# Kernel tuning notes

Hardware: AMD Instinct MI355X
Metric: run time of the kernel (lower is better)

Reference implementation:

```python
import jax, jax.numpy as jnp
import numpy as np

CHANNELS = 512
NUM_HEADS = 8
GROUPS = 8
EPS = 1e-5


def setup_inputs() -> dict:
    key = jax.random.key(0)
    ks = jax.random.split(key, 7)
    c = CHANNELS
    x = jax.random.normal(ks[0], (32, c, 32, 32), dtype=jnp.float32)
    norm_scale = 1.0 + 0.02 * jax.random.normal(ks[1], (c,), dtype=jnp.float32)
    norm_bias = 0.02 * jax.random.normal(ks[2], (c,), dtype=jnp.float32)
    qkv_w = jax.random.normal(ks[3], (3 * c, c), dtype=jnp.float32) / np.sqrt(c).astype(np.float32)
    qkv_b = 0.01 * jax.random.normal(ks[4], (3 * c,), dtype=jnp.float32)
    proj_w = jax.random.normal(ks[5], (c, c), dtype=jnp.float32) / np.sqrt(c).astype(np.float32)
    proj_b = 0.01 * jax.random.normal(ks[6], (c,), dtype=jnp.float32)
    return {"x": x, "norm_scale": norm_scale, "norm_bias": norm_bias,
            "qkv_w": qkv_w, "qkv_b": qkv_b, "proj_w": proj_w, "proj_b": proj_b}


def reference(x, norm_scale, norm_bias, qkv_w, qkv_b, proj_w, proj_b):
    b, c, h, w = x.shape
    heads = NUM_HEADS
    d = c // heads  # head dim
    # GroupNorm(8, c): normalize over (c//groups, h, w) per group
    xg = x.reshape(b, GROUPS, -1)
    mean = xg.mean(axis=-1, keepdims=True)
    var = xg.var(axis=-1, keepdims=True)
    xn = ((xg - mean) * jax.lax.rsqrt(var + EPS)).reshape(b, c, h, w)
    xn = xn * norm_scale[:, None, None] + norm_bias[:, None, None]
    # 1x1 conv == per-pixel GEMM over channels
    qkv = jnp.einsum('bchw,oc->bohw', xn, qkv_w) + qkv_b[:, None, None]
    q, k, v = jnp.split(qkv, 3, axis=1)  # each [b, c, h, w]
    q = q.reshape(b, heads, d, h * w)
    k = k.reshape(b, heads, d, h * w)
    v = v.reshape(b, heads, d, h * w)
    # scores: [b, heads, hw, hw]
    attn = jnp.einsum('bhdn,bhdm->bhnm', q, k) * (d ** -0.5)
    attn = jax.nn.softmax(attn, axis=-1)
    out = jnp.einsum('bhnm,bhdm->bhdn', attn, v).reshape(b, c, h, w)
    out = jnp.einsum('bchw,oc->bohw', out, proj_w) + proj_b[:, None, None]
    return out + x
```

## Files before the change

kernel.cpp:

```cpp
#include <hip/hip_runtime.h>
#include <stdint.h>

typedef float  f32x4  __attribute__((ext_vector_type(4)));
typedef float  f32x16 __attribute__((ext_vector_type(16)));
typedef __bf16 bf16x8 __attribute__((ext_vector_type(8)));
typedef unsigned int   u32;
typedef unsigned int   u32x4v __attribute__((ext_vector_type(4)));
typedef unsigned short u16;

#define DEVI static __device__ __forceinline__

DEVI void gload16(void* lds, const void* g) {
  __builtin_amdgcn_global_load_lds((const __attribute__((address_space(1))) u32*)g,
                                   (__attribute__((address_space(3))) u32*)lds, 16, 0, 0);
}
DEVI f32x4 mfma16(bf16x8 a, bf16x8 b, f32x4 c) {
  return __builtin_amdgcn_mfma_f32_16x16x32_bf16(a, b, c, 0, 0, 0);
}
DEVI f32x16 mfma32(bf16x8 a, bf16x8 b, f32x16 c) {
  return __builtin_amdgcn_mfma_f32_32x32x16_bf16(a, b, c, 0, 0, 0);
}
DEVI u16 f2bf(float f) {
  u32 u = __builtin_bit_cast(u32, f);
  return (u16)((u + 0x7FFFu + ((u >> 16) & 1u)) >> 16);
}
DEVI u32 cvtpk(float lo, float hi) {
  u32 r;
  asm("v_cvt_pk_bf16_f32 %0, %1, %2" : "=v"(r) : "v"(lo), "v"(hi));
  return r;
}
DEVI bf16x8 mkfrag(u32 a, u32 b, u32 c, u32 d) {
  u32x4v u = {a, b, c, d};
  return __builtin_bit_cast(bf16x8, u);
}
#if __has_builtin(__builtin_amdgcn_exp2f)
DEVI float exp2fast(float x) { return __builtin_amdgcn_exp2f(x); }
#else
DEVI float exp2fast(float x) { return exp2f(x); }
#endif

__global__ __launch_bounds__(1024) void k_gn_norm_t(
    const float* __restrict__ x, const float* __restrict__ scale,
    const float* __restrict__ bias, u16* __restrict__ xnT) {
  const int g = blockIdx.x, b = blockIdx.y;
  const float* xg = x + ((size_t)(b*8 + g)) * 65536;
  const int t = threadIdx.x;

  float s = 0.f, ss = 0.f;
  const float4* p4 = (const float4*)xg;
  #pragma unroll
  for (int i = 0; i < 16; i++) {
    float4 v = p4[t + i*1024];
    s  += v.x + v.y + v.z + v.w;
    ss += v.x*v.x + v.y*v.y + v.z*v.z + v.w*v.w;
  }
  #pragma unroll
  for (int off = 32; off; off >>= 1) { s += __shfl_down(s, off); ss += __shfl_down(ss, off); }
  __shared__ float sa[16], sb[16];
  __shared__ float stats[2];
  if ((t & 63) == 0) { sa[t >> 6] = s; sb[t >> 6] = ss; }
  __syncthreads();
  if (t == 0) {
    float S = 0.f, SS = 0.f;
    #pragma unroll
    for (int i = 0; i < 16; i++) { S += sa[i]; SS += sb[i]; }
    float mean = S * (1.f/65536.f);
    float var  = SS * (1.f/65536.f) - mean*mean;
    stats[0] = mean;
    stats[1] = rsqrtf(var + 1e-5f);
  }
  __syncthreads();
  const float mean = stats[0], rstd = stats[1];

  __shared__ __align__(16) char T[4][8192];
  const int grp = t >> 8, lt = t & 255;
  const int n_l = lt & 63;
  for (int it = 0; it < 4; it++) {
    const int n0 = (it*4 + grp) * 64;
    #pragma unroll
    for (int i = 0; i < 16; i++) {
      int c_l = i*4 + (lt >> 6);
      float xv = xg[(size_t)c_l*1024 + n0 + n_l];
      float val = (xv - mean)*rstd*scale[g*64 + c_l] + bias[g*64 + c_l];
      *(u16*)(T[grp] + n_l*128 + ((c_l*2) ^ ((n_l&7)<<4))) = f2bf(val);
    }
    __syncthreads();
    u16* outp = xnT + ((size_t)b*1024 + n0)*512 + g*64;
    #pragma unroll
    for (int i = 0; i < 2; i++) {
      int idx = i*256 + lt;
      int n_ = idx >> 3, sl = idx & 7;
      uint4 val = *(const uint4*)(T[grp] + n_*128 + ((sl ^ (n_&7))<<4));
      *(uint4*)((char*)outp + (size_t)n_*1024 + sl*16) = val;
    }
    __syncthreads();
  }
}

__global__ __launch_bounds__(256) void k_cvt(const float* __restrict__ a,
                                             u16* __restrict__ o, int n) {
  int i = blockIdx.x * 256 + threadIdx.x;
  const int stride = gridDim.x * 256;
  for (; i < n; i += stride) o[i] = f2bf(a[i]);
}

template<int MODE>
__global__ __launch_bounds__(256) void k_gemm(
    const u16* __restrict__ A, const u16* __restrict__ Bt,
    const float* __restrict__ bias, const float* __restrict__ xres,
    u16* __restrict__ oq, u16* __restrict__ ok, u16* __restrict__ ov,
    float* __restrict__ out) {
  __shared__ __align__(16) char lds[65536];
  const int t = threadIdx.x;
  const int wv = t >> 6, ln = t & 63;
  const int wr = wv >> 1, wc = wv & 1;
  const int b  = blockIdx.z;
  const int n0 = blockIdx.x * 128;
  const int m0 = blockIdx.y * 128;
  const u16* Bb = Bt + (size_t)b * (1024*512);

  f32x4 acc[4][4];
  #pragma unroll
  for (int i = 0; i < 4; i++)
    #pragma unroll
    for (int j = 0; j < 4; j++) acc[i][j] = f32x4{0.f,0.f,0.f,0.f};

  const int srow = ln >> 3, ssl = ln & 7;
  const int csw  = ssl ^ (srow & 7);

  auto stage = [&](int buf, int kb) {
    char* base = lds + (buf << 15);
    #pragma unroll
    for (int i = 0; i < 4; i++) {
      int row = wv*32 + i*8 + srow;
      gload16(base + (wv*32 + i*8)*128,
              (const char*)A  + ((size_t)(m0+row)*512 + kb*64)*2 + csw*16);
      gload16(base + 16384 + (wv*32 + i*8)*128,
              (const char*)Bb + ((size_t)(n0+row)*512 + kb*64)*2 + csw*16);
    }
  };

  stage(0, 0);
  __syncthreads();

  for (int kb = 0; kb < 8; kb++) {
    if (kb < 7) stage((kb + 1) & 1, kb + 1);
    const char* cb = lds + ((kb & 1) << 15);
    #pragma unroll
    for (int kf = 0; kf < 2; kf++) {
      bf16x8 af[4], bfr[4];
      #pragma unroll
      for (int mi = 0; mi < 4; mi++) {
        int row = wr*64 + mi*16 + (ln & 15);
        af[mi] = *(const bf16x8*)(cb + row*128 + ((kf*64 + ((ln>>4)<<4)) ^ ((row&7)<<4)));
      }
      #pragma unroll
      for (int ni = 0; ni < 4; ni++) {
        int row = wc*64 + ni*16 + (ln & 15);
        bfr[ni] = *(const bf16x8*)(cb + 16384 + row*128 + ((kf*64 + ((ln>>4)<<4)) ^ ((row&7)<<4)));
      }
      __builtin_amdgcn_s_setprio(1);
      #pragma unroll
      for (int mi = 0; mi < 4; mi++)
        #pragma unroll
        for (int ni = 0; ni < 4; ni++)
          acc[mi][ni] = mfma16(af[mi], bfr[ni], acc[mi][ni]);
      __builtin_amdgcn_s_setprio(0);
    }
    __syncthreads();
  }

  if constexpr (MODE == 0) {
    if (m0 >= 1024) {
      #pragma unroll
      for (int mi = 0; mi < 4; mi++) {
        #pragma unroll
        for (int r = 0; r < 4; r++) {
          int o_l = wr*64 + mi*16 + ((ln>>4)<<2) + r;
          float bia = bias[m0 + o_l];
          size_t rowoff = ((size_t)b*512 + (m0-1024) + o_l)*1024 + n0 + wc*64 + (ln & 15);
          #pragma unroll
          for (int ni = 0; ni < 4; ni++)
            ov[rowoff + ni*16] = f2bf(acc[mi][ni][r] + bia);
        }
      }
    } else {
      const bool isq = (m0 < 512);
      const float sq = isq ? 0.18033688f : 1.0f;
      u16* dstb = isq ? oq : ok;
      const int mloc = isq ? m0 : (m0 - 512);
      #pragma unroll
      for (int mi = 0; mi < 4; mi++) {
        #pragma unroll
        for (int r = 0; r < 4; r++) {
          int o_l = wr*64 + mi*16 + ((ln>>4)<<2) + r;
          float bia = bias[m0 + o_l];
          #pragma unroll
          for (int ni = 0; ni < 4; ni++) {
            int n_l = wc*64 + ni*16 + (ln & 15);
            *(u16*)(lds + n_l*256 + ((o_l*2) ^ ((n_l&7)<<4))) =
                f2bf((acc[mi][ni][r] + bia) * sq);
          }
        }
      }
      __syncthreads();
      const int h0 = mloc >> 6;
      #pragma unroll
      for (int i = 0; i < 8; i++) {
        int idx = i*256 + t;
        int n_ = idx >> 4, s = idx & 15;
        uint4 val = *(const uint4*)(lds + n_*256 + ((s ^ (n_&7))<<4));
        u16* dst = dstb + ((size_t)(b*8 + h0 + (s>>3))*1024 + (n0 + n_))*64 + (s&7)*8;
        *(uint4*)dst = val;
      }
    }
  } else {
    #pragma unroll
    for (int mi = 0; mi < 4; mi++) {
      #pragma unroll
      for (int r = 0; r < 4; r++) {
        int o_l = wr*64 + mi*16 + ((ln>>4)<<2) + r;
        float bia = bias[m0 + o_l];
        size_t rowoff = ((size_t)b*512 + m0 + o_l)*1024 + n0 + wc*64 + (ln & 15);
        #pragma unroll
        for (int ni = 0; ni < 4; ni++)
          out[rowoff + ni*16] = acc[mi][ni][r] + bia + xres[rowoff + ni*16];
      }
    }
  }
}

__global__ __launch_bounds__(512, 4) void k_attn(
    const u16* __restrict__ qT, const u16* __restrict__ kT,
    const u16* __restrict__ v, u16* __restrict__ aoT) {
  __shared__ __align__(16) char lds[65536];
  const int t = threadIdx.x, wv = t >> 6, ln = t & 63;
  const int l31 = ln & 31, hi = ln >> 5;
  const int qt = blockIdx.x, h = blockIdx.y, b = blockIdx.z;
  const size_t bh = (size_t)(b*8 + h);
  const int q0 = qt*256 + wv*32;
  const char* qp = (const char*)qT + (bh*1024 + q0)*128;
  const char* kp = (const char*)kT + bh*1024*128;
  const char* vp = (const char*)v  + bh*64*2048;

  const int srow = ln >> 3;
  const int csw16 = ((ln & 7) ^ srow) << 4;
  const int rsw = (l31 & 7) << 4;
  const int grow = wv*8 + srow;

  auto stageChunk = [&](char* base, int mc) {
    gload16(base + wv*1024,         kp + (size_t)(mc*128 + grow)*128 + csw16);
    gload16(base + 8192 + wv*1024,  kp + (size_t)(mc*128 + 64 + grow)*128 + csw16);
    gload16(base + 16384 + wv*1024, vp + (size_t)grow*2048 + mc*256 + csw16);
    gload16(base + 24576 + wv*1024, vp + (size_t)grow*2048 + mc*256 + 128 + csw16);
  };

  stageChunk(lds, 0);

  bf16x8 qf[4];
  #pragma unroll
  for (int ks = 0; ks < 4; ks++)
    qf[ks] = *(const bf16x8*)(qp + (size_t)l31*128 + ks*32 + hi*16);

  f32x16 zv;
  #pragma unroll
  for (int i = 0; i < 16; i++) zv[i] = 0.f;

  f32x16 o0, o1;
  #pragma unroll
  for (int i = 0; i < 16; i++) { o0[i] = 0.f; o1[i] = 0.f; }
  float M = -1e30f, L = 0.f;

  auto qk = [&](const char* Kl, f32x16& s0, f32x16& s1) {
    __builtin_amdgcn_s_setprio(1);
    {
      int col = (hi*16) ^ rsw;
      bf16x8 k0 = *(const bf16x8*)(Kl + (size_t)l31*128 + col);
      bf16x8 k1 = *(const bf16x8*)(Kl + (size_t)(32 + l31)*128 + col);
      s0 = mfma32(k0, qf[0], zv);
      s1 = mfma32(k1, qf[0], zv);
    }
    #pragma unroll
    for (int ks = 1; ks < 4; ks++) {
      int col = (ks*32 + hi*16) ^ rsw;
      bf16x8 k0 = *(const bf16x8*)(Kl + (size_t)l31*128 + col);
      bf16x8 k1 = *(const bf16x8*)(Kl + (size_t)(32 + l31)*128 + col);
      s0 = mfma32(k0, qf[ks], s0);
      s1 = mfma32(k1, qf[ks], s1);
    }
    __builtin_amdgcn_s_setprio(0);
  };

  auto sm = [&](f32x16& s0, f32x16& s1, bf16x8* pf) {
    float m8[8];
    #pragma unroll
    for (int i = 0; i < 8; i++)
      m8[i] = fmaxf(fmaxf(s0[2*i], s0[2*i+1]), fmaxf(s1[2*i], s1[2*i+1]));
    float m4a = fmaxf(m8[0], m8[1]), m4b = fmaxf(m8[2], m8[3]);
    float m4c = fmaxf(m8[4], m8[5]), m4d = fmaxf(m8[6], m8[7]);
    float cm = fmaxf(fmaxf(m4a, m4b), fmaxf(m4c, m4d));
    cm = fmaxf(cm, __shfl_xor(cm, 32));
    if (!__all(cm <= M + 11.f)) {
      float nm = fmaxf(M, cm);
      float al = exp2fast(M - nm);
      M = nm;
      #pragma unroll
      for (int i = 0; i < 16; i++) { o0[i] *= al; o1[i] *= al; }
      L *= al;
    }
    #pragma unroll
    for (int i = 0; i < 16; i++) {
      s0[i] = exp2fast(s0[i] - M);
      s1[i] = exp2fast(s1[i] - M);
    }
    float r8[8];
    #pragma unroll
    for (int i = 0; i < 8; i++)
      r8[i] = (s0[2*i] + s0[2*i+1]) + (s1[2*i] + s1[2*i+1]);
    float r4a = r8[0] + r8[1], r4b = r8[2] + r8[3];
    float r4c = r8[4] + r8[5], r4d = r8[6] + r8[7];
    L += (r4a + r4b) + (r4c + r4d);

    u32 x0 = cvtpk(s0[0],  s0[1]),  x1 = cvtpk(s0[2],  s0[3]);
    u32 x2 = cvtpk(s0[4],  s0[5]),  x3 = cvtpk(s0[6],  s0[7]);
    u32 x4 = cvtpk(s0[8],  s0[9]),  x5 = cvtpk(s0[10], s0[11]);
    u32 x6 = cvtpk(s0[12], s0[13]), x7 = cvtpk(s0[14], s0[15]);
    u32 y0 = cvtpk(s1[0],  s1[1]),  y1 = cvtpk(s1[2],  s1[3]);
    u32 y2 = cvtpk(s1[4],  s1[5]),  y3 = cvtpk(s1[6],  s1[7]);
    u32 y4 = cvtpk(s1[8],  s1[9]),  y5 = cvtpk(s1[10], s1[11]);
    u32 y6 = cvtpk(s1[12], s1[13]), y7 = cvtpk(s1[14], s1[15]);
    u32 e0 = (u32)__shfl_xor((int)(hi ? x0 : x2), 32);
    u32 e1 = (u32)__shfl_xor((int)(hi ? x1 : x3), 32);
    u32 e2 = (u32)__shfl_xor((int)(hi ? x4 : x6), 32);
    u32 e3 = (u32)__shfl_xor((int)(hi ? x5 : x7), 32);
    u32 f0 = (u32)__shfl_xor((int)(hi ? y0 : y2), 32);
    u32 f1 = (u32)__shfl_xor((int)(hi ? y1 : y3), 32);
    u32 f2 = (u32)__shfl_xor((int)(hi ? y4 : y6), 32);
    u32 f3 = (u32)__shfl_xor((int)(hi ? y5 : y7), 32);
    pf[0] = hi ? mkfrag(e0, e1, x2, x3) : mkfrag(x0, x1, e0, e1);
    pf[1] = hi ? mkfrag(e2, e3, x6, x7) : mkfrag(x4, x5, e2, e3);
    pf[2] = hi ? mkfrag(f0, f1, y2, y3) : mkfrag(y0, y1, f0, f1);
    pf[3] = hi ? mkfrag(f2, f3, y6, y7) : mkfrag(y4, y5, f2, f3);
  };

  auto pv = [&](const char* Vl, const bf16x8* pf) {
    __builtin_amdgcn_s_setprio(1);
    #pragma unroll
    for (int s = 0; s < 4; s++) {
      int col = (s*32 + hi*16) ^ rsw;
      bf16x8 v0 = *(const bf16x8*)(Vl + (size_t)l31*128 + col);
      bf16x8 v1 = *(const bf16x8*)(Vl + (size_t)(32 + l31)*128 + col);
      o0 = mfma32(v0, pf[s], o0);
      o1 = mfma32(v1, pf[s], o1);
    }
    __builtin_amdgcn_s_setprio(0);
  };

  __syncthreads();

  for (int mc = 0; mc < 8; mc++) {
    char* cb = lds + ((mc & 1) << 15);
    if (mc < 7) stageChunk(lds + (((mc + 1) & 1) << 15), mc + 1);
    f32x16 sa0, sa1, sb0, sb1;
    bf16x8 pfA[4], pfB[4];
    qk(cb, sa0, sa1);
    sm(sa0, sa1, pfA);
    qk(cb + 8192, sb0, sb1);
    pv(cb + 16384, pfA);
    sm(sb0, sb1, pfB);
    pv(cb + 24576, pfB);
    __syncthreads();
  }

  L += __shfl_xor(L, 32);
  float inv = 1.f / L;
  u16* dst = aoT + ((size_t)(b*1024 + q0 + l31))*512 + h*64;
  #pragma unroll
  for (int qd = 0; qd < 4; qd++) {
    uint2 val;
    val.x = cvtpk(o0[4*qd+0]*inv, o0[4*qd+1]*inv);
    val.y = cvtpk(o0[4*qd+2]*inv, o0[4*qd+3]*inv);
    *(uint2*)(dst + qd*8 + hi*4) = val;
  }
  #pragma unroll
  for (int qd = 0; qd < 4; qd++) {
    uint2 val;
    val.x = cvtpk(o1[4*qd+0]*inv, o1[4*qd+1]*inv);
    val.y = cvtpk(o1[4*qd+2]*inv, o1[4*qd+3]*inv);
    *(uint2*)(dst + 32 + qd*8 + hi*4) = val;
  }
}

extern "C" void kernel_launch(void* const* d_in, const int* in_sizes, int n_in,
                              void* d_out, int out_size, void* d_ws, size_t ws_size,
                              hipStream_t stream) {
  const float* x     = (const float*)d_in[0];
  const float* nsc   = (const float*)d_in[1];
  const float* nbi   = (const float*)d_in[2];
  const float* qkvw  = (const float*)d_in[3];
  const float* qkvb  = (const float*)d_in[4];
  const float* projw = (const float*)d_in[5];
  const float* projb = (const float*)d_in[6];
  float* out = (float*)d_out;

  char* ws = (char*)d_ws;
  u16* qkvwb  = (u16*)(ws + 2048);
  u16* projwb = (u16*)(ws + 2048 + 1572864);
  char* p = ws + 2048 + 1572864 + 524288;
  u16* qT  = (u16*)p; p += 33554432;
  u16* kTb = (u16*)p; p += 33554432;
  u16* vb  = (u16*)p; p += 33554432;
  u16* xnT = (u16*)p;
  u16* aoT = xnT;

  k_cvt<<<768, 256, 0, stream>>>(qkvw, qkvwb, 1536*512);
  k_cvt<<<256, 256, 0, stream>>>(projw, projwb, 512*512);
  k_gn_norm_t<<<dim3(8, 32), 1024, 0, stream>>>(x, nsc, nbi, xnT);
  k_gemm<0><<<dim3(8, 12, 32), 256, 0, stream>>>(qkvwb, xnT, qkvb, nullptr,
                                                 qT, kTb, vb, nullptr);
  k_attn<<<dim3(4, 8, 32), 512, 0, stream>>>(qT, kTb, vb, aoT);
  k_gemm<1><<<dim3(8, 4, 32), 256, 0, stream>>>(projwb, aoT, projb, x,
                                                nullptr, nullptr, nullptr, out);
}
```

Measured before the change: 236.9 us.

## Merge weight conversion launches, reorder attention grid, precompute LDS offsets

Folds the two weight fp32-to-bf16 conversion kernels into one launch to cut launch overhead. Remaps the attention grid so that blocks sharing the same batch-head are scheduled far apart rather than adjacent (query tile now on the slow grid axis), which changes L2 locality of the K/V reads. Hoists the swizzled LDS row and column offsets out of the QK and PV loops and unrolls those loops by hand. Most of this mirrors what the compiler probably already did, so the main effects are one fewer launch and different block ordering.

```diff
diff --git a/kernel.cpp b/kernel.cpp
--- a/kernel.cpp
+++ b/kernel.cpp
@@ -97,11 +97,16 @@
   }
 }
 
-__global__ __launch_bounds__(256) void k_cvt(const float* __restrict__ a,
-                                             u16* __restrict__ o, int n) {
+__global__ __launch_bounds__(256) void k_cvt2(const float* __restrict__ a1,
+                                              u16* __restrict__ o1, int n1,
+                                              const float* __restrict__ a2,
+                                              u16* __restrict__ o2, int n2) {
   int i = blockIdx.x * 256 + threadIdx.x;
   const int stride = gridDim.x * 256;
-  for (; i < n; i += stride) o[i] = f2bf(a[i]);
+  for (; i < n1 + n2; i += stride) {
+    if (i < n1) o1[i] = f2bf(a1[i]);
+    else        o2[i - n1] = f2bf(a2[i - n1]);
+  }
 }
 
 template<int MODE>
@@ -236,7 +241,8 @@
   __shared__ __align__(16) char lds[65536];
   const int t = threadIdx.x, wv = t >> 6, ln = t & 63;
   const int l31 = ln & 31, hi = ln >> 5;
-  const int qt = blockIdx.x, h = blockIdx.y, b = blockIdx.z;
+  const int bhi = blockIdx.x, qt = blockIdx.y;
+  const int b = bhi >> 3, h = bhi & 7;
   const size_t bh = (size_t)(b*8 + h);
   const int q0 = qt*256 + wv*32;
   const char* qp = (const char*)qT + (bh*1024 + q0)*128;
@@ -247,6 +253,12 @@
   const int csw16 = ((ln & 7) ^ srow) << 4;
   const int rsw = (l31 & 7) << 4;
   const int grow = wv*8 + srow;
+
+  const u32 rA = (u32)l31*128, rB = (u32)(32 + l31)*128;
+  const u32 col0 = (u32)((0*32 + hi*16) ^ rsw);
+  const u32 col1 = (u32)((1*32 + hi*16) ^ rsw);
+  const u32 col2 = (u32)((2*32 + hi*16) ^ rsw);
+  const u32 col3 = (u32)((3*32 + hi*16) ^ rsw);
 
   auto stageChunk = [&](char* base, int mc) {
     gload16(base + wv*1024,         kp + (size_t)(mc*128 + grow)*128 + csw16);
@@ -274,19 +286,28 @@
   auto qk = [&](const char* Kl, f32x16& s0, f32x16& s1) {
     __builtin_amdgcn_s_setprio(1);
     {
-      int col = (hi*16) ^ rsw;
-      bf16x8 k0 = *(const bf16x8*)(Kl + (size_t)l31*128 + col);
-      bf16x8 k1 = *(const bf16x8*)(Kl + (size_t)(32 + l31)*128 + col);
+      bf16x8 k0 = *(const bf16x8*)(Kl + rA + col0);
+      bf16x8 k1 = *(const bf16x8*)(Kl + rB + col0);
       s0 = mfma32(k0, qf[0], zv);
       s1 = mfma32(k1, qf[0], zv);
     }
-    #pragma unroll
-    for (int ks = 1; ks < 4; ks++) {
-      int col = (ks*32 + hi*16) ^ rsw;
-      bf16x8 k0 = *(const bf16x8*)(Kl + (size_t)l31*128 + col);
-      bf16x8 k1 = *(const bf16x8*)(Kl + (size_t)(32 + l31)*128 + col);
-      s0 = mfma32(k0, qf[ks], s0);
-      s1 = mfma32(k1, qf[ks], s1);
+    {
+      bf16x8 k0 = *(const bf16x8*)(Kl + rA + col1);
+      bf16x8 k1 = *(const bf16x8*)(Kl + rB + col1);
+      s0 = mfma32(k0, qf[1], s0);
+      s1 = mfma32(k1, qf[1], s1);
+    }
+    {
+      bf16x8 k0 = *(const bf16x8*)(Kl + rA + col2);
+      bf16x8 k1 = *(const bf16x8*)(Kl + rB + col2);
+      s0 = mfma32(k0, qf[2], s0);
+      s1 = mfma32(k1, qf[2], s1);
+    }
+    {
+      bf16x8 k0 = *(const bf16x8*)(Kl + rA + col3);
+      bf16x8 k1 = *(const bf16x8*)(Kl + rB + col3);
+      s0 = mfma32(k0, qf[3], s0);
+      s1 = mfma32(k1, qf[3], s1);
     }
     __builtin_amdgcn_s_setprio(0);
   };
@@ -345,13 +366,29 @@
 
   auto pv = [&](const char* Vl, const bf16x8* pf) {
     __builtin_amdgcn_s_setprio(1);
-    #pragma unroll
-    for (int s = 0; s < 4; s++) {
-      int col = (s*32 + hi*16) ^ rsw;
-      bf16x8 v0 = *(const bf16x8*)(Vl + (size_t)l31*128 + col);
-      bf16x8 v1 = *(const bf16x8*)(Vl + (size_t)(32 + l31)*128 + col);
-      o0 = mfma32(v0, pf[s], o0);
-      o1 = mfma32(v1, pf[s], o1);
+    {
+      bf16x8 v0 = *(const bf16x8*)(Vl + rA + col0);
+      bf16x8 v1 = *(const bf16x8*)(Vl + rB + col0);
+      o0 = mfma32(v0, pf[0], o0);
+      o1 = mfma32(v1, pf[0], o1);
+    }
+    {
+      bf16x8 v0 = *(const bf16x8*)(Vl + rA + col1);
+      bf16x8 v1 = *(const bf16x8*)(Vl + rB + col1);
+      o0 = mfma32(v0, pf[1], o0);
+      o1 = mfma32(v1, pf[1], o1);
+    }
+    {
+      bf16x8 v0 = *(const bf16x8*)(Vl + rA + col2);
+      bf16x8 v1 = *(const bf16x8*)(Vl + rB + col2);
+      o0 = mfma32(v0, pf[2], o0);
+      o1 = mfma32(v1, pf[2], o1);
+    }
+    {
+      bf16x8 v0 = *(const bf16x8*)(Vl + rA + col3);
+      bf16x8 v1 = *(const bf16x8*)(Vl + rB + col3);
+      o0 = mfma32(v0, pf[3], o0);
+      o1 = mfma32(v1, pf[3], o1);
     }
     __builtin_amdgcn_s_setprio(0);
   };
@@ -413,12 +450,11 @@
   u16* xnT = (u16*)p;
   u16* aoT = xnT;
 
-  k_cvt<<<768, 256, 0, stream>>>(qkvw, qkvwb, 1536*512);
-  k_cvt<<<256, 256, 0, stream>>>(projw, projwb, 512*512);
+  k_cvt2<<<1024, 256, 0, stream>>>(qkvw, qkvwb, 1536*512, projw, projwb, 512*512);
   k_gn_norm_t<<<dim3(8, 32), 1024, 0, stream>>>(x, nsc, nbi, xnT);
   k_gemm<0><<<dim3(8, 12, 32), 256, 0, stream>>>(qkvwb, xnT, qkvb, nullptr,
                                                  qT, kTb, vb, nullptr);
-  k_attn<<<dim3(4, 8, 32), 512, 0, stream>>>(qT, kTb, vb, aoT);
+  k_attn<<<dim3(256, 4), 512, 0, stream>>>(qT, kTb, vb, aoT);
   k_gemm<1><<<dim3(8, 4, 32), 256, 0, stream>>>(projwb, aoT, projb, x,
                                                 nullptr, nullptr, nullptr, out);
 }
```

Result: faster. 231.7 us (-2.2%).
